# Optimization experiments

Hardware: AMD Instinct MI355X
Metric: run time of the kernel (lower is better)

Reference implementation:

```python
import jax, jax.numpy as jnp
import numpy as np

N_NODES = 50000
N_EDGES = 640000
IN_C, HID_C, OUT_C = 64, 128, 64


def _glorot(key, fan_in, fan_out):
    lim = float(np.sqrt(6.0 / (fan_in + fan_out)))
    return jax.random.uniform(key, (fan_in, fan_out), jnp.float32, -lim, lim)


def setup_inputs() -> dict:
    key = jax.random.key(0)
    ks = jax.random.split(key, 16)
    x = jax.random.normal(ks[0], (N_NODES, IN_C), jnp.float32)
    edge_index = jax.random.randint(ks[1], (2, N_EDGES), 0, N_NODES, jnp.int64)
    # SAGEConv params: out = mean_aggr(x_j) @ Wl + x @ Wr + b
    dims = [(IN_C, HID_C), (HID_C, HID_C), (HID_C, OUT_C)]
    params = {}
    for i, (fi, fo) in enumerate(dims):
        params[f"Wl{i}"] = _glorot(ks[2 + 3 * i], fi, fo)
        params[f"Wr{i}"] = _glorot(ks[3 + 3 * i], fi, fo)
        params[f"b{i}"] = jnp.zeros((fo,), jnp.float32)
    # classifier: Linear(64,32) -> ReLU -> Linear(32,1) -> Sigmoid (dropout off in eval)
    params["Wc1"] = _glorot(ks[11], OUT_C, 32)
    params["bc1"] = jnp.zeros((32,), jnp.float32)
    params["Wc2"] = _glorot(ks[12], 32, 1)
    params["bc2"] = jnp.zeros((1,), jnp.float32)
    return {"x": x, "edge_index": edge_index, **params}


def _sage_conv(x, src, dst, Wl, Wr, b):
    # gather neighbor (source) features along edges, mean-aggregate at target
    msgs = x[src]                                                    # [E, C]
    agg = jax.ops.segment_sum(msgs, dst, num_segments=N_NODES)      # [N, C]
    deg = jax.ops.segment_sum(jnp.ones((src.shape[0], 1), x.dtype), dst,
                              num_segments=N_NODES)                 # [N, 1]
    agg = agg / jnp.maximum(deg, 1.0)
    return agg @ Wl + x @ Wr + b


def reference(x, edge_index, Wl0, Wr0, b0, Wl1, Wr1, b1, Wl2, Wr2, b2,
              Wc1, bc1, Wc2, bc2):
    src, dst = edge_index[0], edge_index[1]
    h = jax.nn.relu(_sage_conv(x, src, dst, Wl0, Wr0, b0))
    h = jax.nn.relu(_sage_conv(h, src, dst, Wl1, Wr1, b1))
    h = _sage_conv(h, src, dst, Wl2, Wr2, b2)                       # [N, 64]
    h = jax.nn.relu(h @ Wc1 + bc1)                                  # [N, 32]
    return jax.nn.sigmoid(h @ Wc2 + bc2)                            # [N, 1]
```

## Files before the change

### kernel.cpp

```cpp
#include <hip/hip_runtime.h>
#include <math.h>

#define NN 50000
#define NE 640000
#define CAP 64

typedef short short8 __attribute__((ext_vector_type(8)));
typedef float f32x4  __attribute__((ext_vector_type(4)));

__device__ __forceinline__ unsigned bfr(float f) {
    unsigned u = __float_as_uint(f);
    return (u + 0x7FFFu + ((u >> 16) & 1u)) >> 16;
}
__device__ __forceinline__ unsigned pk2(float a, float b) { return bfr(a) | (bfr(b) << 16); }
__device__ __forceinline__ float bflo(unsigned u) { return __uint_as_float(u << 16); }
__device__ __forceinline__ float bfhi(unsigned u) { return __uint_as_float(u & 0xFFFF0000u); }

__device__ __forceinline__ void packOne(const float* Wl, const float* Wr,
                                        unsigned short* wp, int idx,
                                        int CIN, int COUT) {
    int k = idx / COUT, n = idx % COUT;
    float v = (k < CIN) ? Wl[k * COUT + n] : Wr[(k - CIN) * COUT + n];
    int kt = k >> 5, quad = (k >> 3) & 3, j = k & 7;
    int nt = n >> 4, l16 = n & 15;
    int NT = COUT / 16;
    wp[(((kt * NT + nt) * 64) + quad * 16 + l16) * 8 + j] = (unsigned short)bfr(v);
}

template <int CIN, int COUT, bool RELU, bool CLS>
__device__ __forceinline__ void
fused_layer(const unsigned* __restrict__ Fu, const unsigned short* __restrict__ Fs,
            const int* __restrict__ nbr, const int* __restrict__ cnt,
            const unsigned short* __restrict__ Wpack, const float* __restrict__ bias,
            unsigned short* __restrict__ outp,
            const unsigned short* __restrict__ WpackC, const float* __restrict__ bc1,
            const float* __restrict__ Wc2, const float* __restrict__ bc2,
            float* __restrict__ outf,
            short* __restrict__ lds, int tile, int t) {
    constexpr int RU = CIN / 2;
    constexpr int PC = RU / 16;
    constexpr int RS = CIN + 8;
    constexpr int RSu = RS / 2;
    constexpr int KT = (2 * CIN) / 32;
    constexpr int NT = COUT / 16;
    constexpr int CS = 136;

    const int g = t >> 4, lg = t & 15;
    const int wave = t >> 6, lane = t & 63;
    const int quad = lane >> 4, l16 = lane & 15;

#pragma unroll 1
    for (int i = 0; i < 8; ++i) {
        const int rloc = g * 8 + i;
        const int gw = tile * 128 + rloc;
        unsigned* lrow = (unsigned*)lds + rloc * RSu + lg * PC;
        if (gw < NN) {
            const int deg = cnt[gw];
            const int m = (deg < CAP) ? deg : CAP;
            float a[2 * PC] = {};
            for (int base = 0; base < m; base += 16) {
                int idx = NN;
                if (base + lg < m) idx = nbr[gw * CAP + base + lg];
#pragma unroll
                for (int j = 0; j < 16; ++j) {
                    const int n = __shfl(idx, j, 16);
                    if (PC == 2) {
                        const uint2 u = *(const uint2*)(Fu + (size_t)n * RU + lg * 2);
                        a[0] += bflo(u.x); a[1] += bfhi(u.x);
                        a[2] += bflo(u.y); a[3] += bfhi(u.y);
                    } else {
                        const uint4 u = *(const uint4*)(Fu + (size_t)n * RU + lg * 4);
                        a[0] += bflo(u.x); a[1] += bfhi(u.x);
                        a[2] += bflo(u.y); a[3] += bfhi(u.y);
                        a[4] += bflo(u.z); a[5] += bfhi(u.z);
                        a[6] += bflo(u.w); a[7] += bfhi(u.w);
                    }
                }
            }
            const float di = 1.0f / (float)((deg > 1) ? deg : 1);
            if (PC == 2)
                *(uint2*)lrow = make_uint2(pk2(a[0] * di, a[1] * di),
                                           pk2(a[2] * di, a[3] * di));
            else
                *(uint4*)lrow = make_uint4(pk2(a[0] * di, a[1] * di),
                                           pk2(a[2] * di, a[3] * di),
                                           pk2(a[4] * di, a[5] * di),
                                           pk2(a[6] * di, a[7] * di));
        } else {
            if (PC == 2) *(uint2*)lrow = make_uint2(0u, 0u);
            else         *(uint4*)lrow = make_uint4(0u, 0u, 0u, 0u);
        }
    }
    __syncthreads();

    const int rbase = tile * 128 + wave * 32;
    int r0 = rbase + l16;      if (r0 >= NN) r0 = NN - 1;
    int r1 = rbase + 16 + l16; if (r1 >= NN) r1 = NN - 1;
    const int rl0 = wave * 32 + l16, rl1 = rl0 + 16;

    f32x4 acc[2][NT] = {};
#pragma unroll
    for (int kt = 0; kt < KT; ++kt) {
        short8 a0, a1;
        if (kt < KT / 2) {
            a0 = *(const short8*)(lds + rl0 * RS + kt * 32 + quad * 8);
            a1 = *(const short8*)(lds + rl1 * RS + kt * 32 + quad * 8);
        } else {
            a0 = *(const short8*)(Fs + (size_t)r0 * CIN + (kt * 32 - CIN) + quad * 8);
            a1 = *(const short8*)(Fs + (size_t)r1 * CIN + (kt * 32 - CIN) + quad * 8);
        }
#pragma unroll
        for (int nt = 0; nt < NT; ++nt) {
            const short8 bfrag = *(const short8*)(Wpack + (size_t)((kt * NT + nt) * 64 + lane) * 8);
            acc[0][nt] = __builtin_amdgcn_mfma_f32_16x16x32_bf16(a0, bfrag, acc[0][nt], 0, 0, 0);
            acc[1][nt] = __builtin_amdgcn_mfma_f32_16x16x32_bf16(a1, bfrag, acc[1][nt], 0, 0, 0);
        }
    }
    __syncthreads();

    if constexpr (!CLS) {
#pragma unroll
        for (int nt = 0; nt < NT; ++nt) {
            const float bb = bias[nt * 16 + l16];
#pragma unroll
            for (int s = 0; s < 2; ++s)
#pragma unroll
                for (int rg = 0; rg < 4; ++rg) {
                    const int rloc = wave * 32 + s * 16 + quad * 4 + rg;
                    float v = acc[s][nt][rg] + bb;
                    if (RELU) v = fmaxf(v, 0.f);
                    lds[rloc * CS + nt * 16 + l16] = (short)(unsigned short)bfr(v);
                }
        }
        __syncthreads();
        constexpr int CH = COUT / 8;
        for (int idx = t; idx < 128 * CH; idx += 256) {
            const int row = idx / CH, c8 = idx % CH;
            const int gr = tile * 128 + row;
            if (gr < NN)
                *(uint4*)(outp + (size_t)gr * COUT + c8 * 8) =
                    *(const uint4*)(lds + row * CS + c8 * 8);
        }
    } else {
        constexpr int HS = 72;
#pragma unroll
        for (int nt = 0; nt < NT; ++nt) {
            const float bb = bias[nt * 16 + l16];
#pragma unroll
            for (int s = 0; s < 2; ++s)
#pragma unroll
                for (int rg = 0; rg < 4; ++rg) {
                    const int rloc = wave * 32 + s * 16 + quad * 4 + rg;
                    lds[rloc * HS + nt * 16 + l16] =
                        (short)(unsigned short)bfr(acc[s][nt][rg] + bb);
                }
        }
        __syncthreads();

        f32x4 sacc[2][2] = {};
#pragma unroll
        for (int s = 0; s < 2; ++s) {
            const int rloc = wave * 32 + s * 16 + l16;
#pragma unroll
            for (int kt2 = 0; kt2 < 2; ++kt2) {
                const short8 af = *(const short8*)(lds + rloc * HS + kt2 * 32 + quad * 8);
#pragma unroll
                for (int nt2 = 0; nt2 < 2; ++nt2) {
                    const short8 bf = *(const short8*)(WpackC + (size_t)((kt2 * 2 + nt2) * 64 + lane) * 8);
                    sacc[s][nt2] = __builtin_amdgcn_mfma_f32_16x16x32_bf16(af, bf, sacc[s][nt2], 0, 0, 0);
                }
            }
        }

        const float b1a = bc1[l16], b1b = bc1[16 + l16];
        const float w2a = Wc2[l16], w2b = Wc2[16 + l16];
        const float b2v = bc2[0];
#pragma unroll
        for (int s = 0; s < 2; ++s)
#pragma unroll
            for (int rg = 0; rg < 4; ++rg) {
                float p = fmaxf(sacc[s][0][rg] + b1a, 0.f) * w2a +
                          fmaxf(sacc[s][1][rg] + b1b, 0.f) * w2b;
#pragma unroll
                for (int off = 1; off < 16; off <<= 1) p += __shfl_xor(p, off);
                if (l16 == 0) {
                    const int row = tile * 128 + wave * 32 + s * 16 + quad * 4 + rg;
                    if (row < NN) outf[row] = 1.0f / (1.0f + expf(-(p + b2v)));
                }
            }
    }
}

template <int CIN, int COUT, bool RELU, bool CLS>
__global__ __launch_bounds__(256) void
k_fused(const unsigned* __restrict__ Fu, const unsigned short* __restrict__ Fs,
        const int* __restrict__ nbr, const int* __restrict__ cnt,
        const unsigned short* __restrict__ Wpack, const float* __restrict__ bias,
        unsigned short* __restrict__ outp,
        const unsigned short* __restrict__ WpackC, const float* __restrict__ bc1,
        const float* __restrict__ Wc2, const float* __restrict__ bc2,
        float* __restrict__ outf) {
    __shared__ __align__(16) short lds[128 * 136];
    fused_layer<CIN, COUT, RELU, CLS>(Fu, Fs, nbr, cnt, Wpack, bias, outp,
                                      WpackC, bc1, Wc2, bc2, outf,
                                      lds, blockIdx.x, threadIdx.x);
}

__global__ __launch_bounds__(256) void
k_prep(const int* __restrict__ src, const int* __restrict__ dst,
       int* __restrict__ cnt, int* __restrict__ nbr,
       const float* __restrict__ x, unsigned* __restrict__ xb,
       const float* Wl0, const float* Wr0, const float* Wl1, const float* Wr1,
       const float* Wl2, const float* Wr2, const float* Wc1,
       unsigned short* wp0, unsigned short* wp1, unsigned short* wp2,
       unsigned short* wpc, unsigned short* h0b, unsigned short* h1b) {
    const int b = blockIdx.x, t = threadIdx.x;
    if (b < 2500) {
        int e = b * 256 + t;
        if (e < NE) {
            int d = dst[e];
            int p = atomicAdd(&cnt[d], 1);
            if (p < CAP) nbr[d * CAP + p] = src[e];
        }
        if (b == 0) {
            if (t < 32) xb[(size_t)NN * 32 + t] = 0u;
            else if (t < 96) ((unsigned*)h0b)[(size_t)NN * 64 + (t - 32)] = 0u;
            else if (t < 160) ((unsigned*)h1b)[(size_t)NN * 64 + (t - 96)] = 0u;
        }
    } else if (b < 5625) {
        int i = (b - 2500) * 256 + t;
        if (i < NN * 16) {
            float4 v = ((const float4*)x)[i];
            ((uint2*)xb)[i] = make_uint2(pk2(v.x, v.y), pk2(v.z, v.w));
        }
    } else {
        int idx = (b - 5625) * 256 + t;
        if (idx < 16384) packOne(Wl0, Wr0, wp0, idx, 64, 128);
        else if (idx < 49152) packOne(Wl1, Wr1, wp1, idx - 16384, 128, 128);
        else if (idx < 65536) packOne(Wl2, Wr2, wp2, idx - 49152, 128, 64);
        else if (idx < 67584) packOne(Wc1, Wc1, wpc, idx - 65536, 64, 32);
    }
}

extern "C" void kernel_launch(void* const* d_in, const int* in_sizes, int n_in,
                              void* d_out, int out_size, void* d_ws, size_t ws_size,
                              hipStream_t stream) {
    const float* x   = (const float*)d_in[0];
    const int*   ei  = (const int*)d_in[1];
    const int*   src = ei;
    const int*   dst = ei + NE;
    const float* Wl0 = (const float*)d_in[2];
    const float* Wr0 = (const float*)d_in[3];
    const float* b0  = (const float*)d_in[4];
    const float* Wl1 = (const float*)d_in[5];
    const float* Wr1 = (const float*)d_in[6];
    const float* b1  = (const float*)d_in[7];
    const float* Wl2 = (const float*)d_in[8];
    const float* Wr2 = (const float*)d_in[9];
    const float* b2  = (const float*)d_in[10];
    const float* Wc1 = (const float*)d_in[11];
    const float* bc1 = (const float*)d_in[12];
    const float* Wc2 = (const float*)d_in[13];
    const float* bc2 = (const float*)d_in[14];
    float* out = (float*)d_out;

    char*  ws   = (char*)d_ws;
    int*   cnt  = (int*)(ws);
    unsigned short* wp0 = (unsigned short*)(ws + (size_t)256 * 1024);
    unsigned short* wp1 = (unsigned short*)(ws + (size_t)352 * 1024);
    unsigned short* wp2 = (unsigned short*)(ws + (size_t)448 * 1024);
    unsigned short* wpc = (unsigned short*)(ws + (size_t)512 * 1024);
    int*   nbr  = (int*)(ws + (size_t)1 * (1 << 20));
    unsigned short* xb   = (unsigned short*)(ws + (size_t)16 * (1 << 20));
    unsigned short* h0b  = (unsigned short*)(ws + (size_t)40 * (1 << 20));
    unsigned short* h1b  = (unsigned short*)(ws + (size_t)56 * (1 << 20));

    hipMemsetAsync(cnt, 0, (size_t)NN * sizeof(int), stream);

    const int B = 256;
    const int NTILE = (NN + 127) / 128;

    k_prep<<<5889, B, 0, stream>>>(src, dst, cnt, nbr, x, (unsigned*)xb,
                                   Wl0, Wr0, Wl1, Wr1, Wl2, Wr2, Wc1,
                                   wp0, wp1, wp2, wpc, h0b, h1b);

    k_fused<64, 128, true, false><<<NTILE, B, 0, stream>>>(
        (const unsigned*)xb, xb, nbr, cnt, wp0, b0, h0b,
        nullptr, nullptr, nullptr, nullptr, nullptr);

    k_fused<128, 128, true, false><<<NTILE, B, 0, stream>>>(
        (const unsigned*)h0b, h0b, nbr, cnt, wp1, b1, h1b,
        nullptr, nullptr, nullptr, nullptr, nullptr);

    k_fused<128, 64, false, true><<<NTILE, B, 0, stream>>>(
        (const unsigned*)h1b, h1b, nbr, cnt, wp2, b2, nullptr,
        wpc, bc1, Wc2, bc2, out);
}
```

Baseline: 235.9 us.

## Halve node tile to 64 rows and batch neighbor gathers before accumulation

The node tile per block shrinks from 128 to 64 rows, so each wave computes one 16-row MFMA strip instead of two. This doubles the grid size and halves LDS per block, which should give more blocks per CU and better latency hiding for the gather-heavy phase. The neighbor gather loop now issues all 16 loads into a register array before accumulating, exposing memory-level parallelism. The cost is higher register pressure from the u[16] array and more weight-fragment reloads per row across blocks.

```diff
diff --git a/kernel.cpp b/kernel.cpp
--- a/kernel.cpp
+++ b/kernel.cpp
@@ -4,6 +4,7 @@
 #define NN 50000
 #define NE 640000
 #define CAP 64
+#define TM 64
 
 typedef short short8 __attribute__((ext_vector_type(8)));
 typedef float f32x4  __attribute__((ext_vector_type(4)));
@@ -50,9 +51,9 @@
     const int quad = lane >> 4, l16 = lane & 15;
 
 #pragma unroll 1
-    for (int i = 0; i < 8; ++i) {
-        const int rloc = g * 8 + i;
-        const int gw = tile * 128 + rloc;
+    for (int i = 0; i < TM / 16; ++i) {
+        const int rloc = g * (TM / 16) + i;
+        const int gw = tile * TM + rloc;
         unsigned* lrow = (unsigned*)lds + rloc * RSu + lg * PC;
         if (gw < NN) {
             const int deg = cnt[gw];
@@ -61,19 +62,31 @@
             for (int base = 0; base < m; base += 16) {
                 int idx = NN;
                 if (base + lg < m) idx = nbr[gw * CAP + base + lg];
-#pragma unroll
-                for (int j = 0; j < 16; ++j) {
-                    const int n = __shfl(idx, j, 16);
-                    if (PC == 2) {
-                        const uint2 u = *(const uint2*)(Fu + (size_t)n * RU + lg * 2);
-                        a[0] += bflo(u.x); a[1] += bfhi(u.x);
-                        a[2] += bflo(u.y); a[3] += bfhi(u.y);
-                    } else {
-                        const uint4 u = *(const uint4*)(Fu + (size_t)n * RU + lg * 4);
-                        a[0] += bflo(u.x); a[1] += bfhi(u.x);
-                        a[2] += bflo(u.y); a[3] += bfhi(u.y);
-                        a[4] += bflo(u.z); a[5] += bfhi(u.z);
-                        a[6] += bflo(u.w); a[7] += bfhi(u.w);
+                if (PC == 2) {
+                    uint2 u[16];
+#pragma unroll
+                    for (int j = 0; j < 16; ++j) {
+                        const int n = __shfl(idx, j, 16);
+                        u[j] = *(const uint2*)(Fu + (size_t)n * RU + lg * 2);
+                    }
+#pragma unroll
+                    for (int j = 0; j < 16; ++j) {
+                        a[0] += bflo(u[j].x); a[1] += bfhi(u[j].x);
+                        a[2] += bflo(u[j].y); a[3] += bfhi(u[j].y);
+                    }
+                } else {
+                    uint4 u[16];
+#pragma unroll
+                    for (int j = 0; j < 16; ++j) {
+                        const int n = __shfl(idx, j, 16);
+                        u[j] = *(const uint4*)(Fu + (size_t)n * RU + lg * 4);
+                    }
+#pragma unroll
+                    for (int j = 0; j < 16; ++j) {
+                        a[0] += bflo(u[j].x); a[1] += bfhi(u[j].x);
+                        a[2] += bflo(u[j].y); a[3] += bfhi(u[j].y);
+                        a[4] += bflo(u[j].z); a[5] += bfhi(u[j].z);
+                        a[6] += bflo(u[j].w); a[7] += bfhi(u[j].w);
                     }
                 }
             }
@@ -93,27 +106,22 @@
     }
     __syncthreads();
 
-    const int rbase = tile * 128 + wave * 32;
-    int r0 = rbase + l16;      if (r0 >= NN) r0 = NN - 1;
-    int r1 = rbase + 16 + l16; if (r1 >= NN) r1 = NN - 1;
-    const int rl0 = wave * 32 + l16, rl1 = rl0 + 16;
-
-    f32x4 acc[2][NT] = {};
+    const int rbase = tile * TM + wave * 16;
+    int r0 = rbase + l16; if (r0 >= NN) r0 = NN - 1;
+    const int rl0 = wave * 16 + l16;
+
+    f32x4 acc[NT] = {};
 #pragma unroll
     for (int kt = 0; kt < KT; ++kt) {
-        short8 a0, a1;
-        if (kt < KT / 2) {
+        short8 a0;
+        if (kt < KT / 2)
             a0 = *(const short8*)(lds + rl0 * RS + kt * 32 + quad * 8);
-            a1 = *(const short8*)(lds + rl1 * RS + kt * 32 + quad * 8);
-        } else {
+        else
             a0 = *(const short8*)(Fs + (size_t)r0 * CIN + (kt * 32 - CIN) + quad * 8);
-            a1 = *(const short8*)(Fs + (size_t)r1 * CIN + (kt * 32 - CIN) + quad * 8);
-        }
 #pragma unroll
         for (int nt = 0; nt < NT; ++nt) {
             const short8 bfrag = *(const short8*)(Wpack + (size_t)((kt * NT + nt) * 64 + lane) * 8);
-            acc[0][nt] = __builtin_amdgcn_mfma_f32_16x16x32_bf16(a0, bfrag, acc[0][nt], 0, 0, 0);
-            acc[1][nt] = __builtin_amdgcn_mfma_f32_16x16x32_bf16(a1, bfrag, acc[1][nt], 0, 0, 0);
+            acc[nt] = __builtin_amdgcn_mfma_f32_16x16x32_bf16(a0, bfrag, acc[nt], 0, 0, 0);
         }
     }
     __syncthreads();
@@ -123,20 +131,18 @@
         for (int nt = 0; nt < NT; ++nt) {
             const float bb = bias[nt * 16 + l16];
 #pragma unroll
-            for (int s = 0; s < 2; ++s)
-#pragma unroll
-                for (int rg = 0; rg < 4; ++rg) {
-                    const int rloc = wave * 32 + s * 16 + quad * 4 + rg;
-                    float v = acc[s][nt][rg] + bb;
-                    if (RELU) v = fmaxf(v, 0.f);
-                    lds[rloc * CS + nt * 16 + l16] = (short)(unsigned short)bfr(v);
-                }
+            for (int rg = 0; rg < 4; ++rg) {
+                const int rloc = wave * 16 + quad * 4 + rg;
+                float v = acc[nt][rg] + bb;
+                if (RELU) v = fmaxf(v, 0.f);
+                lds[rloc * CS + nt * 16 + l16] = (short)(unsigned short)bfr(v);
+            }
         }
         __syncthreads();
         constexpr int CH = COUT / 8;
-        for (int idx = t; idx < 128 * CH; idx += 256) {
+        for (int idx = t; idx < TM * CH; idx += 256) {
             const int row = idx / CH, c8 = idx % CH;
-            const int gr = tile * 128 + row;
+            const int gr = tile * TM + row;
             if (gr < NN)
                 *(uint4*)(outp + (size_t)gr * COUT + c8 * 8) =
                     *(const uint4*)(lds + row * CS + c8 * 8);
@@ -147,28 +153,23 @@
         for (int nt = 0; nt < NT; ++nt) {
             const float bb = bias[nt * 16 + l16];
 #pragma unroll
-            for (int s = 0; s < 2; ++s)
-#pragma unroll
-                for (int rg = 0; rg < 4; ++rg) {
-                    const int rloc = wave * 32 + s * 16 + quad * 4 + rg;
-                    lds[rloc * HS + nt * 16 + l16] =
-                        (short)(unsigned short)bfr(acc[s][nt][rg] + bb);
-                }
+            for (int rg = 0; rg < 4; ++rg) {
+                const int rloc = wave * 16 + quad * 4 + rg;
+                lds[rloc * HS + nt * 16 + l16] =
+                    (short)(unsigned short)bfr(acc[nt][rg] + bb);
+            }
         }
         __syncthreads();
 
-        f32x4 sacc[2][2] = {};
-#pragma unroll
-        for (int s = 0; s < 2; ++s) {
-            const int rloc = wave * 32 + s * 16 + l16;
-#pragma unroll
-            for (int kt2 = 0; kt2 < 2; ++kt2) {
-                const short8 af = *(const short8*)(lds + rloc * HS + kt2 * 32 + quad * 8);
-#pragma unroll
-                for (int nt2 = 0; nt2 < 2; ++nt2) {
-                    const short8 bf = *(const short8*)(WpackC + (size_t)((kt2 * 2 + nt2) * 64 + lane) * 8);
-                    sacc[s][nt2] = __builtin_amdgcn_mfma_f32_16x16x32_bf16(af, bf, sacc[s][nt2], 0, 0, 0);
-                }
+        f32x4 sacc[2] = {};
+        const int rloc = wave * 16 + l16;
+#pragma unroll
+        for (int kt2 = 0; kt2 < 2; ++kt2) {
+            const short8 af = *(const short8*)(lds + rloc * HS + kt2 * 32 + quad * 8);
+#pragma unroll
+            for (int nt2 = 0; nt2 < 2; ++nt2) {
+                const short8 bf = *(const short8*)(WpackC + (size_t)((kt2 * 2 + nt2) * 64 + lane) * 8);
+                sacc[nt2] = __builtin_amdgcn_mfma_f32_16x16x32_bf16(af, bf, sacc[nt2], 0, 0, 0);
             }
         }
 
@@ -176,18 +177,16 @@
         const float w2a = Wc2[l16], w2b = Wc2[16 + l16];
         const float b2v = bc2[0];
 #pragma unroll
-        for (int s = 0; s < 2; ++s)
-#pragma unroll
-            for (int rg = 0; rg < 4; ++rg) {
-                float p = fmaxf(sacc[s][0][rg] + b1a, 0.f) * w2a +
-                          fmaxf(sacc[s][1][rg] + b1b, 0.f) * w2b;
-#pragma unroll
-                for (int off = 1; off < 16; off <<= 1) p += __shfl_xor(p, off);
-                if (l16 == 0) {
-                    const int row = tile * 128 + wave * 32 + s * 16 + quad * 4 + rg;
-                    if (row < NN) outf[row] = 1.0f / (1.0f + expf(-(p + b2v)));
-                }
-            }
+        for (int rg = 0; rg < 4; ++rg) {
+            float p = fmaxf(sacc[0][rg] + b1a, 0.f) * w2a +
+                      fmaxf(sacc[1][rg] + b1b, 0.f) * w2b;
+#pragma unroll
+            for (int off = 1; off < 16; off <<= 1) p += __shfl_xor(p, off);
+            if (l16 == 0) {
+                const int row = tile * TM + wave * 16 + quad * 4 + rg;
+                if (row < NN) outf[row] = 1.0f / (1.0f + expf(-(p + b2v)));
+            }
+        }
     }
 }
 
@@ -200,7 +199,7 @@
         const unsigned short* __restrict__ WpackC, const float* __restrict__ bc1,
         const float* __restrict__ Wc2, const float* __restrict__ bc2,
         float* __restrict__ outf) {
-    __shared__ __align__(16) short lds[128 * 136];
+    __shared__ __align__(16) short lds[TM * 136];
     fused_layer<CIN, COUT, RELU, CLS>(Fu, Fs, nbr, cnt, Wpack, bias, outp,
                                       WpackC, bc1, Wc2, bc2, outf,
                                       lds, blockIdx.x, threadIdx.x);
@@ -278,7 +277,7 @@
     hipMemsetAsync(cnt, 0, (size_t)NN * sizeof(int), stream);
 
     const int B = 256;
-    const int NTILE = (NN + 127) / 128;
+    const int NTILE = (NN + TM - 1) / TM;
 
     k_prep<<<5889, B, 0, stream>>>(src, dst, cnt, nbr, x, (unsigned*)xb,
                                    Wl0, Wr0, Wl1, Wr1, Wl2, Wr2, Wc1,
```

Result: faster. 216.9 us (-8.1%).
